# Optimization experiments

Measured on AMD Instinct MI355X. Metric: run time of the kernel, lower is better.

Reference implementation:

```python
import jax, jax.numpy as jnp
import numpy as np

H, G, D = 16, 4, 64  # heads, n_global, head_dim
DM = H * D           # 1024 hidden size
B, N = 8, 4096


def setup_inputs() -> dict:
    key = jax.random.key(0)
    ks = jax.random.split(key, 16)
    std = 0.02
    def lin(k, fi, fo):
        return jax.random.normal(k, (fi, fo), dtype=jnp.float32) * std
    return {
        "hidden_states": jax.random.normal(ks[0], (B, N, DM), dtype=jnp.float32),
        "attention_mask": jnp.zeros((B, 1, N), dtype=jnp.float32),
        "Wq": lin(ks[1], DM, DM), "bq": jnp.zeros((DM,), jnp.float32),
        "Wqa": lin(ks[2], DM, H * G), "bqa": jnp.zeros((H * G,), jnp.float32),
        "Wk": lin(ks[3], DM, DM), "bk": jnp.zeros((DM,), jnp.float32),
        "Wka": lin(ks[4], DM, H * G), "bka": jnp.zeros((H * G,), jnp.float32),
        "Wv": lin(ks[5], DM, DM), "bv": jnp.zeros((DM,), jnp.float32),
        "Wt": lin(ks[6], DM, DM), "bt": jnp.zeros((DM,), jnp.float32),
    }


def reference(hidden_states, attention_mask, Wq, bq, Wqa, bqa, Wk, bk, Wka, bka, Wv, bv, Wt, bt):
    b, n, _ = hidden_states.shape
    scale = D ** 0.5
    q = hidden_states @ Wq + bq            # b n (h d)
    k = hidden_states @ Wk + bk
    v = hidden_states @ Wv + bv
    # query attention scores: b n (h g) -> b h g n
    qs = (q @ Wqa + bqa).reshape(b, n, H, G).transpose(0, 2, 3, 1) / scale
    qs = qs + attention_mask[:, None]      # broadcast over h (and g)
    qw = jax.nn.softmax(qs, axis=-1)       # b h g n
    mq = q.reshape(b, n, H, D).transpose(0, 2, 1, 3)   # b h n d
    gq = jnp.einsum('bhgn,bhnd->bhdg', qw, mq)          # b h d g
    kh = k.reshape(b, n, H, D).transpose(0, 2, 1, 3)    # b h n d
    qk = kh[..., None] * gq[:, :, None]                 # b h n d g
    qk = qk.transpose(0, 2, 1, 3, 4).reshape(b, n, H * D, G)
    qk = jnp.max(qk, axis=-1)                           # b n (h d)
    # NOTE: original code adds mask but does NOT softmax this score
    ksc = (qk @ Wka + bka).reshape(b, n, H, G).transpose(0, 2, 3, 1) / scale
    ksc = ksc + attention_mask[:, None]                 # b h g n
    gk = jnp.einsum('bhgn,bhnd->bhdg', ksc, kh)         # b h d g
    vh = v.reshape(b, n, H, D).transpose(0, 2, 1, 3)    # b h n d
    u = gk[:, :, None] * vh[..., None]                  # b h n d g
    u = jnp.max(u, axis=-1)                             # b h n d
    u = u.transpose(0, 2, 1, 3).reshape(b, n, H * D)    # b n (h d)
    r = u @ Wt + bt
    return r + q
```

## Files before the change

kernel.cpp:

```cpp
#include <hip/hip_runtime.h>
#include <hip/hip_bf16.h>

typedef __bf16 bf16;
typedef __attribute__((ext_vector_type(8))) __bf16 bf16x8;
typedef __attribute__((ext_vector_type(4))) float floatx4;


__device__ __forceinline__ void gload_lds16(const void* g, void* l) {
    __builtin_amdgcn_global_load_lds(
        (const __attribute__((address_space(1))) unsigned int*)g,
        (__attribute__((address_space(3))) unsigned int*)l, 16, 0, 0);
}

__global__ __launch_bounds__(256)
void cvt_kernel(const float* __restrict__ src, bf16* __restrict__ dst, int n8) {
    int i8 = blockIdx.x * 256 + threadIdx.x;
    if (i8 >= n8) return;
    const float* s = src + (size_t)i8 * 8;
    float4 x = *(const float4*)s;
    float4 y = *(const float4*)(s + 4);
    bf16x8 o;
    o[0] = (bf16)x.x; o[1] = (bf16)x.y; o[2] = (bf16)x.z; o[3] = (bf16)x.w;
    o[4] = (bf16)y.x; o[5] = (bf16)y.y; o[6] = (bf16)y.z; o[7] = (bf16)y.w;
    *(bf16x8*)(dst + (size_t)i8 * 8) = o;
}

__global__ __launch_bounds__(256)
void transpose_cvt_kernel(const float* __restrict__ src, bf16* __restrict__ dst, int R, int C) {
    __shared__ bf16 tile[64][65];
    int tr0 = blockIdx.x * 64;
    int tc0 = blockIdx.y * 64;
    int tx = threadIdx.x & 63, ty = threadIdx.x >> 6;
#pragma unroll
    for (int j = 0; j < 16; j++) {
        int r = ty + j * 4;
        tile[tx][r] = (bf16)src[(size_t)(tr0 + r) * C + tc0 + tx];
    }
    __syncthreads();
#pragma unroll
    for (int j = 0; j < 16; j++) {
        int r = ty + j * 4;
        dst[(size_t)(tc0 + r) * R + tr0 + tx] = tile[r][tx];
    }
}

__global__ __launch_bounds__(256)
void biaspack_kernel(const float* __restrict__ bq, const float* __restrict__ bk,
                     const float* __restrict__ bv, float* __restrict__ biasf,
                     float* __restrict__ zbias) {
    int i = blockIdx.x * 256 + threadIdx.x;
    if (i < 1024)      biasf[i] = bq[i];
    else if (i < 2048) biasf[i] = bk[i - 1024];
    else if (i < 3072) biasf[i] = bv[i - 2048];
    else if (i < 3200) biasf[i] = 0.f;
    else if (i < 4224) zbias[i - 3200] = 0.f;
}

__global__ __launch_bounds__(64)
void compbias_kernel(const float* __restrict__ bq, const float* __restrict__ Wqa,
                     const float* __restrict__ bqa, float* __restrict__ out) {
    int j = threadIdx.x;
    float a = 0.f;
    for (int t = 0; t < 1024; t++) a += bq[t] * Wqa[(size_t)t * 64 + j];
    out[j] = a + bqa[j];
}

template<int BN, int WN, int EPI>
__global__ __launch_bounds__(WN * 128)
void gemm_kernel(const bf16* __restrict__ A, int lda,
                 const bf16* __restrict__ WT,
                 const float* __restrict__ bias,
                 void* __restrict__ Cout, int ldc,
                 const float* __restrict__ mask,
                 const bf16* __restrict__ qadd, int ldq,
                 int K) {
    constexpr int BM = 128;
    constexpr int NT = WN * 128;
    __shared__ bf16 As[BM * 32];
    __shared__ bf16 Bs[BN * 32];

    const int tid  = threadIdx.x;
    const int wid  = tid >> 6;
    const int lane = tid & 63;
    const int l16  = lane & 15;
    const int quad = lane >> 4;
    const int wm   = wid & 1;
    const int wn   = wid >> 1;
    const int m0   = blockIdx.x * BM;
    const int n0   = blockIdx.y * BN;

    floatx4 acc[4][4];
#pragma unroll
    for (int i = 0; i < 4; i++)
#pragma unroll
        for (int j = 0; j < 4; j++) acc[i][j] = (floatx4)0.0f;

    for (int k0 = 0; k0 < K; k0 += 32) {
        __syncthreads();
#pragma unroll
        for (int i = tid; i < BM * 4; i += NT) {
            const bf16* gp = A + (size_t)(m0 + (i >> 2)) * lda + k0 + (i & 3) * 8;
            gload_lds16(gp, (char*)As + (size_t)(i & ~63) * 16);
        }
#pragma unroll
        for (int i = tid; i < BN * 4; i += NT) {
            const bf16* gp = WT + (size_t)(n0 + (i >> 2)) * K + k0 + (i & 3) * 8;
            gload_lds16(gp, (char*)Bs + (size_t)(i & ~63) * 16);
        }
        __syncthreads();
        bf16x8 af[4], bfv[4];
#pragma unroll
        for (int mi = 0; mi < 4; mi++)
            af[mi] = *(const bf16x8*)&As[(wm * 64 + mi * 16 + l16) * 32 + quad * 8];
#pragma unroll
        for (int ni = 0; ni < 4; ni++)
            bfv[ni] = *(const bf16x8*)&Bs[(wn * 64 + ni * 16 + l16) * 32 + quad * 8];
#pragma unroll
        for (int mi = 0; mi < 4; mi++)
#pragma unroll
            for (int ni = 0; ni < 4; ni++)
                acc[mi][ni] = __builtin_amdgcn_mfma_f32_16x16x32_bf16(
                    af[mi], bfv[ni], acc[mi][ni], 0, 0, 0);
    }

#pragma unroll
    for (int mi = 0; mi < 4; mi++) {
#pragma unroll
        for (int ni = 0; ni < 4; ni++) {
            int col  = n0 + wn * 64 + ni * 16 + l16;
            int rowb = m0 + wm * 64 + mi * 16 + quad * 4;
            float bv = bias[col];
#pragma unroll
            for (int e = 0; e < 4; e++) {
                int row = rowb + e;
                float v = acc[mi][ni][e] + bv;
                if (EPI == 0) {
                    ((bf16*)Cout)[(size_t)row * ldc + col] = (bf16)v;
                } else if (EPI == 2) {
                    ((float*)Cout)[(size_t)row * ldc + col] = v * 0.125f + mask[row];
                } else {
                    v += (float)qadd[(size_t)row * ldq + col];
                    ((float*)Cout)[(size_t)row * ldc + col] = v;
                }
            }
        }
    }
}

__global__ __launch_bounds__(256)
void softmax_kernel(const bf16* __restrict__ qkv, const float* __restrict__ mask,
                    float* __restrict__ qw) {
    int bh = blockIdx.x;
    int b = bh >> 6, hg = bh & 63;
    int tid = threadIdx.x;
    float xs[16];
    float mx = -1e30f;
#pragma unroll
    for (int j = 0; j < 16; j++) {
        int n = tid + j * 256;
        float x = (float)qkv[(size_t)(b * 4096 + n) * 3200 + 3072 + hg] * 0.125f
                  + mask[b * 4096 + n];
        xs[j] = x;
        mx = fmaxf(mx, x);
    }
    __shared__ float red[256];
    red[tid] = mx;
    __syncthreads();
    for (int s = 128; s > 0; s >>= 1) {
        if (tid < s) red[tid] = fmaxf(red[tid], red[tid + s]);
        __syncthreads();
    }
    mx = red[0];
    __syncthreads();
    float sum = 0.f;
#pragma unroll
    for (int j = 0; j < 16; j++) { xs[j] = __expf(xs[j] - mx); sum += xs[j]; }
    red[tid] = sum;
    __syncthreads();
    for (int s = 128; s > 0; s >>= 1) {
        if (tid < s) red[tid] += red[tid + s];
        __syncthreads();
    }
    float inv = 1.0f / red[0];
#pragma unroll
    for (int j = 0; j < 16; j++)
        qw[(size_t)bh * 4096 + tid + j * 256] = xs[j] * inv;
}

__global__ __launch_bounds__(256)
void gq1_kernel(const float* __restrict__ qw, const bf16* __restrict__ qkv,
                float* __restrict__ part) {
    int bh = blockIdx.x, ch = blockIdx.y;
    int b = bh >> 4, h = bh & 15;
    int tid = threadIdx.x;
    int g = tid >> 6, d = tid & 63;
    const float* wrow = qw + ((size_t)(b * 64 + h * 4 + g)) * 4096 + ch * 256;
    const bf16* qcol  = qkv + (size_t)(b * 4096 + ch * 256) * 3200 + h * 64 + d;
    float a = 0.f;
#pragma unroll 8
    for (int n = 0; n < 256; n++)
        a += wrow[n] * (float)qcol[(size_t)n * 3200];
    part[(((size_t)bh * 16 + ch) * 4 + g) * 64 + d] = a;
}

__global__ __launch_bounds__(256)
void gk1_kernel(const float* __restrict__ ksc, const bf16* __restrict__ qkv,
                float* __restrict__ part) {
    int bh = blockIdx.x, ch = blockIdx.y;
    int b = bh >> 4, h = bh & 15;
    int tid = threadIdx.x;
    int g = tid >> 6, d = tid & 63;
    const float* sbase = ksc + (size_t)(b * 4096 + ch * 256) * 64 + h * 4 + g;
    const bf16* kcol   = qkv + (size_t)(b * 4096 + ch * 256) * 3200 + 1024 + h * 64 + d;
    float a = 0.f;
#pragma unroll 8
    for (int n = 0; n < 256; n++)
        a += sbase[(size_t)n * 64] * (float)kcol[(size_t)n * 3200];
    part[(((size_t)bh * 16 + ch) * 4 + g) * 64 + d] = a;
}

__global__ __launch_bounds__(256)
void gred_kernel(const float* __restrict__ part,
                 float* __restrict__ gmax, float* __restrict__ gmin) {
    int bh = blockIdx.x;
    int tid = threadIdx.x;
    int g = tid >> 6, d = tid & 63;
    float a = 0.f;
#pragma unroll
    for (int c = 0; c < 16; c++)
        a += part[(((size_t)bh * 16 + c) * 4 + g) * 64 + d];
    __shared__ float sg[4][64];
    sg[g][d] = a;
    __syncthreads();
    if (tid < 64) {
        float mx = sg[0][tid], mn = sg[0][tid];
#pragma unroll
        for (int gg = 1; gg < 4; gg++) {
            mx = fmaxf(mx, sg[gg][tid]);
            mn = fminf(mn, sg[gg][tid]);
        }
        gmax[bh * 64 + tid] = mx;
        gmin[bh * 64 + tid] = mn;
    }
}

__global__ __launch_bounds__(256)
void maxg_kernel(const bf16* __restrict__ qkv, int coloff,
                 const float* __restrict__ gmax, const float* __restrict__ gmin,
                 bf16* __restrict__ dst) {
    size_t i8 = (size_t)blockIdx.x * 256 + threadIdx.x;
    size_t e0 = i8 * 8;
    int row = (int)(e0 >> 10);
    int c   = (int)(e0 & 1023);
    int b   = row >> 12;
    bf16x8 kv = *(const bf16x8*)(qkv + (size_t)row * 3200 + coloff + c);
    bf16x8 out;
#pragma unroll
    for (int j = 0; j < 8; j++) {
        float f  = (float)kv[j];
        float gm = gmax[b * 1024 + c + j];
        float gn = gmin[b * 1024 + c + j];
        out[j] = (bf16)(f >= 0.f ? f * gm : f * gn);
    }
    *(bf16x8*)(dst + e0) = out;
}

extern "C" void kernel_launch(void* const* d_in, const int* in_sizes, int n_in,
                              void* d_out, int out_size, void* d_ws, size_t ws_size,
                              hipStream_t stream) {
    const float* hs   = (const float*)d_in[0];
    const float* mask = (const float*)d_in[1];
    const float* Wq   = (const float*)d_in[2];
    const float* bq   = (const float*)d_in[3];
    const float* Wqa  = (const float*)d_in[4];
    const float* bqa  = (const float*)d_in[5];
    const float* Wk   = (const float*)d_in[6];
    const float* bk   = (const float*)d_in[7];
    const float* Wka  = (const float*)d_in[8];
    const float* bka  = (const float*)d_in[9];
    const float* Wv   = (const float*)d_in[10];
    const float* bv   = (const float*)d_in[11];
    const float* Wt   = (const float*)d_in[12];
    const float* bt   = (const float*)d_in[13];

    char* p = (char*)d_ws;
    auto alloc = [&](size_t bytes) {
        char* r = p;
        p += (bytes + 255) & ~(size_t)255;
        return (void*)r;
    };
    bf16*  WT    = (bf16*) alloc((size_t)3200 * 1024 * 2);
    bf16*  WqBf  = (bf16*) alloc((size_t)1024 * 1024 * 2);
    bf16*  WqaT  = (bf16*) alloc((size_t)128 * 1024 * 2);
    bf16*  WkaT  = (bf16*) alloc((size_t)64 * 1024 * 2);
    bf16*  WtT   = (bf16*) alloc((size_t)1024 * 1024 * 2);
    float* biasf = (float*)alloc((size_t)3200 * 4);
    float* zbias = (float*)alloc((size_t)1024 * 4);
    bf16*  qkv   = (bf16*) alloc((size_t)32768 * 3200 * 2);
    bf16*  hsb   = (bf16*) alloc((size_t)32768 * 1024 * 2);
    float* qw    = (float*)alloc((size_t)512 * 4096 * 4);
    float* part  = (float*)alloc((size_t)128 * 16 * 256 * 4);
    float* gqmax = (float*)alloc((size_t)8192 * 4);
    float* gqmin = (float*)alloc((size_t)8192 * 4);
    float* gkmax = (float*)alloc((size_t)8192 * 4);
    float* gkmin = (float*)alloc((size_t)8192 * 4);
    bf16*  qk_u  = hsb;
    float* ksc   = qw;

    cvt_kernel<<<16384, 256, 0, stream>>>(hs, hsb, 4194304);
    cvt_kernel<<<512, 256, 0, stream>>>(Wq, WqBf, 131072);
    transpose_cvt_kernel<<<dim3(16, 16), 256, 0, stream>>>(Wq, WT, 1024, 1024);
    transpose_cvt_kernel<<<dim3(16, 16), 256, 0, stream>>>(Wk, WT + (size_t)1024 * 1024, 1024, 1024);
    transpose_cvt_kernel<<<dim3(16, 16), 256, 0, stream>>>(Wv, WT + (size_t)2048 * 1024, 1024, 1024);
    transpose_cvt_kernel<<<dim3(16, 1), 256, 0, stream>>>(Wqa, WqaT, 1024, 64);
    transpose_cvt_kernel<<<dim3(16, 1), 256, 0, stream>>>(Wka, WkaT, 1024, 64);
    transpose_cvt_kernel<<<dim3(16, 16), 256, 0, stream>>>(Wt, WtT, 1024, 1024);
    biaspack_kernel<<<17, 256, 0, stream>>>(bq, bk, bv, biasf, zbias);
    compbias_kernel<<<1, 64, 0, stream>>>(bq, Wqa, bqa, biasf + 3072);
    gemm_kernel<128, 2, 0><<<dim3(1, 8), 256, 0, stream>>>(
        WqaT, 1024, WqBf, zbias, WT + (size_t)3072 * 1024, 1024, nullptr, nullptr, 0, 1024);

    gemm_kernel<128, 2, 0><<<dim3(256, 25), 256, 0, stream>>>(
        hsb, 1024, WT, biasf, qkv, 3200, nullptr, nullptr, 0, 1024);
    softmax_kernel<<<512, 256, 0, stream>>>(qkv, mask, qw);
    gq1_kernel<<<dim3(128, 16), 256, 0, stream>>>(qw, qkv, part);
    gred_kernel<<<128, 256, 0, stream>>>(part, gqmax, gqmin);
    maxg_kernel<<<16384, 256, 0, stream>>>(qkv, 1024, gqmax, gqmin, qk_u);
    gemm_kernel<64, 1, 2><<<dim3(256, 1), 128, 0, stream>>>(
        qk_u, 1024, WkaT, bka, ksc, 64, mask, nullptr, 0, 1024);
    gk1_kernel<<<dim3(128, 16), 256, 0, stream>>>(ksc, qkv, part);
    gred_kernel<<<128, 256, 0, stream>>>(part, gkmax, gkmin);
    maxg_kernel<<<16384, 256, 0, stream>>>(qkv, 2048, gkmax, gkmin, qk_u);
    gemm_kernel<128, 2, 3><<<dim3(256, 8), 256, 0, stream>>>(
        qk_u, 1024, WtT, bt, d_out, 1024, nullptr, qkv, 3200, 1024);
}
```

Measured before the change: 988.2 us.

## Add 256x256 double-buffered MFMA GEMM with interleaved staging for big projections

Adds a new 512-thread GEMM kernel with 256x256 output tiles, 128KB of dynamic LDS double buffering, direct global-to-LDS loads interleaved between MFMA phases, explicit waitcnt and barriers, s_setprio around the MFMA blocks, and an XCD-aware block swizzle. It replaces the 128-tile GEMM for the fused QKV projection and for the output projection. The larger tiles raise data reuse and cut global traffic, and the schedule hides load latency. The QKV weight buffer is padded to 3328 rows because the N tiles overrun 3200 columns, and the padding rows are read but never initialised. The hand-written barrier and waitcnt schedule is fragile.

```diff
diff --git a/kernel.cpp b/kernel.cpp
--- a/kernel.cpp
+++ b/kernel.cpp
@@ -11,6 +11,9 @@
         (const __attribute__((address_space(1))) unsigned int*)g,
         (__attribute__((address_space(3))) unsigned int*)l, 16, 0, 0);
 }
+
+#define WAIT_LGKM0() asm volatile("s_waitcnt lgkmcnt(0)" ::: "memory")
+#define WAIT_VM(N) asm volatile("s_waitcnt vmcnt(" #N ")" ::: "memory")
 
 __global__ __launch_bounds__(256)
 void cvt_kernel(const float* __restrict__ src, bf16* __restrict__ dst, int n8) {
@@ -141,6 +144,163 @@
                 } else {
                     v += (float)qadd[(size_t)row * ldq + col];
                     ((float*)Cout)[(size_t)row * ldc + col] = v;
+                }
+            }
+        }
+    }
+}
+
+#define DO_MFMA(MH, NH)                                                              \
+    _Pragma("unroll")                                                                \
+    for (int r_ = 0; r_ < 4; ++r_) {                                                 \
+        _Pragma("unroll")                                                            \
+        for (int nj_ = 0; nj_ < 2; ++nj_) {                                          \
+            _Pragma("unroll")                                                        \
+            for (int kk_ = 0; kk_ < 2; ++kk_) {                                      \
+                acc[(MH) * 4 + r_][(NH) * 2 + nj_] =                                 \
+                    __builtin_amdgcn_mfma_f32_16x16x32_bf16(                         \
+                        af[r_][kk_], bfv[(NH) * 2 + nj_][kk_],                       \
+                        acc[(MH) * 4 + r_][(NH) * 2 + nj_], 0, 0, 0);                \
+            }                                                                        \
+        }                                                                            \
+    }
+
+template<int EPI>
+__global__ __launch_bounds__(512, 2)
+void gemm256_kernel(const bf16* __restrict__ A, int lda,
+                    const bf16* __restrict__ B, int ldb,
+                    const float* __restrict__ bias,
+                    void* __restrict__ Cout, int ldc, int ncols,
+                    const bf16* __restrict__ qadd, int ldq,
+                    int K, int ntn) {
+    extern __shared__ __align__(16) char smem[];
+    const int tid  = threadIdx.x;
+    const int wid  = tid >> 6;
+    const int lane = tid & 63;
+    const int l16  = lane & 15;
+    const int quad = lane >> 4;
+    const int wm   = wid >> 2;
+    const int wn   = wid & 3;
+
+    const int nwg  = gridDim.x * gridDim.y;
+    const int orig = blockIdx.y * gridDim.x + blockIdx.x;
+    int swz = orig;
+    if ((nwg & 7) == 0) swz = (orig & 7) * (nwg >> 3) + (orig >> 3);
+    const int m0 = (swz / ntn) * 256;
+    const int n0 = (swz % ntn) * 256;
+
+    const int NT = K >> 6;
+
+    const int lrow = lane >> 2;
+    const int lcb8 = ((lane & 3) ^ ((lane >> 5) << 1)) << 3;
+    const int aoff = (l16 * 64 + quad * 16) ^ ((l16 & 8) << 2);
+
+    auto stage = [&](const bf16* __restrict__ base, int ldx, int r0,
+                     int kt, int h, int lbase) {
+#pragma unroll
+        for (int j = 0; j < 2; ++j) {
+            int rg_l = j * 4 + (wid >> 1);
+            int cg   = wid & 1;
+            const bf16* gp = base + (size_t)(r0 + h * 128 + rg_l * 16 + lrow) * ldx
+                             + (kt << 6) + (cg << 5) + lcb8;
+            char* lp = smem + lbase + ((kt & 1) << 15)
+                       + (((h * 8 + rg_l) * 2 + cg) << 10);
+            gload_lds16(gp, lp);
+        }
+    };
+
+    floatx4 acc[8][4];
+#pragma unroll
+    for (int i = 0; i < 8; ++i)
+#pragma unroll
+        for (int j = 0; j < 4; ++j) acc[i][j] = (floatx4)0.0f;
+
+    stage(B, ldb, n0, 0, 0, 65536);
+    stage(B, ldb, n0, 0, 1, 65536);
+    stage(A, lda, m0, 0, 0, 0);
+    stage(A, lda, m0, 0, 1, 0);
+    stage(B, ldb, n0, 1, 0, 65536);
+    stage(B, ldb, n0, 1, 1, 65536);
+    WAIT_VM(4);
+    __builtin_amdgcn_s_barrier();
+
+    for (int t = 0; t < NT; ++t) {
+        const int bsel = (t & 1) << 15;
+        bf16x8 af[4][2], bfv[4][2];
+
+#pragma unroll
+        for (int r = 0; r < 4; ++r)
+#pragma unroll
+            for (int kk = 0; kk < 2; ++kk)
+                af[r][kk] = *(const bf16x8*)(smem + bsel
+                              + (((wm * 8 + r) * 2 + kk) << 10) + aoff);
+#pragma unroll
+        for (int ni = 0; ni < 4; ++ni)
+#pragma unroll
+            for (int kk = 0; kk < 2; ++kk)
+                bfv[ni][kk] = *(const bf16x8*)(smem + 65536 + bsel
+                              + (((wn * 4 + ni) * 2 + kk) << 10) + aoff);
+        if (t + 1 < NT) stage(A, lda, m0, t + 1, 0, 0);
+        __builtin_amdgcn_s_barrier();
+        WAIT_LGKM0();
+        __builtin_amdgcn_s_setprio(1);
+        DO_MFMA(0, 0)
+        __builtin_amdgcn_s_setprio(0);
+        __builtin_amdgcn_s_barrier();
+
+        if (t + 1 < NT) stage(A, lda, m0, t + 1, 1, 0);
+        __builtin_amdgcn_s_barrier();
+        __builtin_amdgcn_s_setprio(1);
+        DO_MFMA(0, 1)
+        __builtin_amdgcn_s_setprio(0);
+        __builtin_amdgcn_s_barrier();
+
+#pragma unroll
+        for (int r = 0; r < 4; ++r)
+#pragma unroll
+            for (int kk = 0; kk < 2; ++kk)
+                af[r][kk] = *(const bf16x8*)(smem + bsel
+                              + (((wm * 8 + 4 + r) * 2 + kk) << 10) + aoff);
+        if (t + 2 < NT) stage(B, ldb, n0, t + 2, 0, 65536);
+        __builtin_amdgcn_s_barrier();
+        WAIT_LGKM0();
+        __builtin_amdgcn_s_setprio(1);
+        DO_MFMA(1, 0)
+        __builtin_amdgcn_s_setprio(0);
+        __builtin_amdgcn_s_barrier();
+
+        if (t + 2 < NT) stage(B, ldb, n0, t + 2, 1, 65536);
+        __builtin_amdgcn_s_barrier();
+        __builtin_amdgcn_s_setprio(1);
+        DO_MFMA(1, 1)
+        __builtin_amdgcn_s_setprio(0);
+        if (t < NT - 2) {
+            WAIT_VM(4);
+            __builtin_amdgcn_s_barrier();
+        } else if (t == NT - 2) {
+            WAIT_VM(0);
+            __builtin_amdgcn_s_barrier();
+        }
+    }
+
+#pragma unroll
+    for (int mi = 0; mi < 8; ++mi) {
+#pragma unroll
+        for (int ni = 0; ni < 4; ++ni) {
+            int col  = n0 + wn * 64 + ni * 16 + l16;
+            int rowb = m0 + wm * 128 + mi * 16 + quad * 4;
+            if (col < ncols) {
+                float bv = bias[col];
+#pragma unroll
+                for (int e = 0; e < 4; ++e) {
+                    int row = rowb + e;
+                    float v = acc[mi][ni][e] + bv;
+                    if (EPI == 0) {
+                        ((bf16*)Cout)[(size_t)row * ldc + col] = (bf16)v;
+                    } else {
+                        v += (float)qadd[(size_t)row * ldq + col];
+                        ((float*)Cout)[(size_t)row * ldc + col] = v;
+                    }
                 }
             }
         }
@@ -289,7 +449,7 @@
         p += (bytes + 255) & ~(size_t)255;
         return (void*)r;
     };
-    bf16*  WT    = (bf16*) alloc((size_t)3200 * 1024 * 2);
+    bf16*  WT    = (bf16*) alloc((size_t)3328 * 1024 * 2);
     bf16*  WqBf  = (bf16*) alloc((size_t)1024 * 1024 * 2);
     bf16*  WqaT  = (bf16*) alloc((size_t)128 * 1024 * 2);
     bf16*  WkaT  = (bf16*) alloc((size_t)64 * 1024 * 2);
@@ -307,6 +467,11 @@
     bf16*  qk_u  = hsb;
     float* ksc   = qw;
 
+    (void)hipFuncSetAttribute(reinterpret_cast<const void*>(&gemm256_kernel<0>),
+                              hipFuncAttributeMaxDynamicSharedMemorySize, 131072);
+    (void)hipFuncSetAttribute(reinterpret_cast<const void*>(&gemm256_kernel<3>),
+                              hipFuncAttributeMaxDynamicSharedMemorySize, 131072);
+
     cvt_kernel<<<16384, 256, 0, stream>>>(hs, hsb, 4194304);
     cvt_kernel<<<512, 256, 0, stream>>>(Wq, WqBf, 131072);
     transpose_cvt_kernel<<<dim3(16, 16), 256, 0, stream>>>(Wq, WT, 1024, 1024);
@@ -320,8 +485,8 @@
     gemm_kernel<128, 2, 0><<<dim3(1, 8), 256, 0, stream>>>(
         WqaT, 1024, WqBf, zbias, WT + (size_t)3072 * 1024, 1024, nullptr, nullptr, 0, 1024);
 
-    gemm_kernel<128, 2, 0><<<dim3(256, 25), 256, 0, stream>>>(
-        hsb, 1024, WT, biasf, qkv, 3200, nullptr, nullptr, 0, 1024);
+    gemm256_kernel<0><<<dim3(128, 13), 512, 131072, stream>>>(
+        hsb, 1024, WT, 1024, biasf, qkv, 3200, 3200, nullptr, 0, 1024, 13);
     softmax_kernel<<<512, 256, 0, stream>>>(qkv, mask, qw);
     gq1_kernel<<<dim3(128, 16), 256, 0, stream>>>(qw, qkv, part);
     gred_kernel<<<128, 256, 0, stream>>>(part, gqmax, gqmin);
@@ -331,6 +496,6 @@
     gk1_kernel<<<dim3(128, 16), 256, 0, stream>>>(ksc, qkv, part);
     gred_kernel<<<128, 256, 0, stream>>>(part, gkmax, gkmin);
     maxg_kernel<<<16384, 256, 0, stream>>>(qkv, 2048, gkmax, gkmin, qk_u);
-    gemm_kernel<128, 2, 3><<<dim3(256, 8), 256, 0, stream>>>(
-        qk_u, 1024, WtT, bt, d_out, 1024, nullptr, qkv, 3200, 1024);
-}
+    gemm256_kernel<3><<<dim3(128, 4), 512, 131072, stream>>>(
+        qk_u, 1024, WtT, 1024, bt, d_out, 1024, 1024, qkv, 3200, 1024, 4);
+}
```

After: 936.0 us. 5.3% less time.

## Add 256x256-tile 8-wave pipelined GEMM for QKV and output projections

Applied to the files above, without the earlier changes.

Adds a new bf16 MFMA GEMM using 256x256 output tiles with 512 threads, a 4-stage LDS ring filled by direct global-to-LDS loads, interleaved half-tile MFMA with explicit vmcnt waits and barriers, setprio around compute, and an XCD-aware block swizzle. The two large projection GEMMs (QKV and final output) use it in place of the 128-tile kernel. The aim is more data reuse per tile and better overlap of loads with MFMA. The weight buffer is padded to 3328 rows so the 13th column tile can read past 3200, and stores are masked by column. Costs are 128KB of LDS per block and more registers, which limits occupancy.

```diff
diff --git a/kernel.cpp b/kernel.cpp
--- a/kernel.cpp
+++ b/kernel.cpp
@@ -11,6 +11,8 @@
         (const __attribute__((address_space(1))) unsigned int*)g,
         (__attribute__((address_space(3))) unsigned int*)l, 16, 0, 0);
 }
+
+#define WAIT_VM(N) asm volatile("s_waitcnt vmcnt(" #N ")" ::: "memory")
 
 __global__ __launch_bounds__(256)
 void cvt_kernel(const float* __restrict__ src, bf16* __restrict__ dst, int n8) {
@@ -141,6 +143,120 @@
                 } else {
                     v += (float)qadd[(size_t)row * ldq + col];
                     ((float*)Cout)[(size_t)row * ldc + col] = v;
+                }
+            }
+        }
+    }
+}
+
+#define STG_A(KT) do { \
+    gload_lds16(gA0 + (KT) * 32, sA + (((KT) & 3) << 14)); \
+    gload_lds16(gA1 + (KT) * 32, sA + (((KT) & 3) << 14) + 1024); } while (0)
+#define STG_B(KT) do { \
+    gload_lds16(gB0 + (KT) * 32, sB + (((KT) & 3) << 14)); \
+    gload_lds16(gB1 + (KT) * 32, sB + (((KT) & 3) << 14) + 1024); } while (0)
+#define RD_AFA(T) { _Pragma("unroll") for (int r_ = 0; r_ < 4; ++r_) \
+    af_a[r_] = *(const bf16x8*)(lA + (((T) & 3) << 14) + r_ * 1024); }
+#define RD_AFB(T) { _Pragma("unroll") for (int r_ = 0; r_ < 4; ++r_) \
+    af_b[r_] = *(const bf16x8*)(lA + (((T) & 3) << 14) + 4096 + r_ * 1024); }
+#define RD_BFV(T, S) { _Pragma("unroll") for (int n_ = 0; n_ < 4; ++n_) \
+    bfv[S][n_] = *(const bf16x8*)(lB + (((T) & 3) << 14) + n_ * 1024); }
+#define MM_HALF(MH, S) { _Pragma("unroll") for (int r_ = 0; r_ < 4; ++r_) \
+    _Pragma("unroll") for (int n_ = 0; n_ < 4; ++n_) \
+    acc[(MH) * 4 + r_][n_] = __builtin_amdgcn_mfma_f32_16x16x32_bf16( \
+        (MH) ? af_b[r_] : af_a[r_], bfv[S][n_], acc[(MH) * 4 + r_][n_], 0, 0, 0); }
+
+template<int EPI>
+__global__ __launch_bounds__(512, 2)
+void gemm256_kernel(const bf16* __restrict__ A, int lda,
+                    const bf16* __restrict__ B, int ldb,
+                    const float* __restrict__ bias,
+                    void* __restrict__ Cout, int ldc, int ncols,
+                    const bf16* __restrict__ qadd, int ldq,
+                    int ntn) {
+    constexpr int NT = 32;
+    extern __shared__ __align__(16) char smem[];
+    const int tid  = threadIdx.x;
+    const int wid  = tid >> 6;
+    const int lane = tid & 63;
+    const int l16  = lane & 15;
+    const int quad = lane >> 4;
+    const int wm   = wid >> 2;
+    const int wn   = wid & 3;
+
+    const int nwg  = gridDim.x * gridDim.y;
+    const int orig = blockIdx.y * gridDim.x + blockIdx.x;
+    int swz = orig;
+    if ((nwg & 7) == 0) swz = (orig & 7) * (nwg >> 3) + (orig >> 3);
+    const int m0 = (swz / ntn) * 256;
+    const int n0 = (swz % ntn) * 256;
+
+    const int srow = wid * 32 + (lane >> 2);
+    const int scol = ((lane & 3) ^ ((lane >> 5) << 1)) << 3;
+    const bf16* gA0 = A + (size_t)(m0 + srow) * lda + scol;
+    const bf16* gA1 = gA0 + (size_t)16 * lda;
+    const bf16* gB0 = B + (size_t)(n0 + srow) * ldb + scol;
+    const bf16* gB1 = gB0 + (size_t)16 * ldb;
+    char* sA = smem + wid * 2048;
+    char* sB = smem + 65536 + wid * 2048;
+    const int aoff = (l16 * 64 + quad * 16) ^ ((l16 & 8) << 2);
+    const char* lA = smem + wm * 8192 + aoff;
+    const char* lB = smem + 65536 + wn * 4096 + aoff;
+
+    floatx4 acc[8][4];
+#pragma unroll
+    for (int i = 0; i < 8; ++i)
+#pragma unroll
+        for (int j = 0; j < 4; ++j) acc[i][j] = (floatx4)0.0f;
+
+    bf16x8 af_a[4], af_b[4], bfv[2][4];
+
+    STG_A(0); STG_B(0); STG_A(1); STG_B(1); STG_A(2); STG_B(2);
+    WAIT_VM(8);
+    __builtin_amdgcn_s_barrier();
+    RD_AFA(0);
+    RD_BFV(0, 0);
+
+#pragma unroll
+    for (int t = 0; t < NT; ++t) {
+        RD_AFB(t);
+        if (t + 3 < NT) STG_A(t + 3);
+        __builtin_amdgcn_s_barrier();
+        __builtin_amdgcn_s_setprio(1);
+        MM_HALF(0, t & 1);
+        __builtin_amdgcn_s_setprio(0);
+        if (t < NT - 3)       { WAIT_VM(6); }
+        else if (t == NT - 3) { WAIT_VM(4); }
+        else if (t == NT - 2) { WAIT_VM(0); }
+        __builtin_amdgcn_s_barrier();
+
+        if (t + 1 < NT) { RD_AFA(t + 1); RD_BFV(t + 1, (t + 1) & 1); }
+        if (t + 3 < NT) STG_B(t + 3);
+        __builtin_amdgcn_s_barrier();
+        __builtin_amdgcn_s_setprio(1);
+        MM_HALF(1, t & 1);
+        __builtin_amdgcn_s_setprio(0);
+        __builtin_amdgcn_s_barrier();
+    }
+
+#pragma unroll
+    for (int mi = 0; mi < 8; ++mi) {
+#pragma unroll
+        for (int ni = 0; ni < 4; ++ni) {
+            int col  = n0 + wn * 64 + ni * 16 + l16;
+            int rowb = m0 + wm * 128 + mi * 16 + quad * 4;
+            if (col < ncols) {
+                float bv = bias[col];
+#pragma unroll
+                for (int e = 0; e < 4; ++e) {
+                    int row = rowb + e;
+                    float v = acc[mi][ni][e] + bv;
+                    if (EPI == 0) {
+                        ((bf16*)Cout)[(size_t)row * ldc + col] = (bf16)v;
+                    } else {
+                        v += (float)qadd[(size_t)row * ldq + col];
+                        ((float*)Cout)[(size_t)row * ldc + col] = v;
+                    }
                 }
             }
         }
@@ -289,7 +405,7 @@
         p += (bytes + 255) & ~(size_t)255;
         return (void*)r;
     };
-    bf16*  WT    = (bf16*) alloc((size_t)3200 * 1024 * 2);
+    bf16*  WT    = (bf16*) alloc((size_t)3328 * 1024 * 2);
     bf16*  WqBf  = (bf16*) alloc((size_t)1024 * 1024 * 2);
     bf16*  WqaT  = (bf16*) alloc((size_t)128 * 1024 * 2);
     bf16*  WkaT  = (bf16*) alloc((size_t)64 * 1024 * 2);
@@ -307,6 +423,11 @@
     bf16*  qk_u  = hsb;
     float* ksc   = qw;
 
+    (void)hipFuncSetAttribute(reinterpret_cast<const void*>(&gemm256_kernel<0>),
+                              hipFuncAttributeMaxDynamicSharedMemorySize, 131072);
+    (void)hipFuncSetAttribute(reinterpret_cast<const void*>(&gemm256_kernel<3>),
+                              hipFuncAttributeMaxDynamicSharedMemorySize, 131072);
+
     cvt_kernel<<<16384, 256, 0, stream>>>(hs, hsb, 4194304);
     cvt_kernel<<<512, 256, 0, stream>>>(Wq, WqBf, 131072);
     transpose_cvt_kernel<<<dim3(16, 16), 256, 0, stream>>>(Wq, WT, 1024, 1024);
@@ -320,8 +441,8 @@
     gemm_kernel<128, 2, 0><<<dim3(1, 8), 256, 0, stream>>>(
         WqaT, 1024, WqBf, zbias, WT + (size_t)3072 * 1024, 1024, nullptr, nullptr, 0, 1024);
 
-    gemm_kernel<128, 2, 0><<<dim3(256, 25), 256, 0, stream>>>(
-        hsb, 1024, WT, biasf, qkv, 3200, nullptr, nullptr, 0, 1024);
+    gemm256_kernel<0><<<dim3(128, 13), 512, 131072, stream>>>(
+        hsb, 1024, WT, 1024, biasf, qkv, 3200, 3200, nullptr, 0, 13);
     softmax_kernel<<<512, 256, 0, stream>>>(qkv, mask, qw);
     gq1_kernel<<<dim3(128, 16), 256, 0, stream>>>(qw, qkv, part);
     gred_kernel<<<128, 256, 0, stream>>>(part, gqmax, gqmin);
@@ -331,6 +452,6 @@
     gk1_kernel<<<dim3(128, 16), 256, 0, stream>>>(ksc, qkv, part);
     gred_kernel<<<128, 256, 0, stream>>>(part, gkmax, gkmin);
     maxg_kernel<<<16384, 256, 0, stream>>>(qkv, 2048, gkmax, gkmin, qk_u);
-    gemm_kernel<128, 2, 3><<<dim3(256, 8), 256, 0, stream>>>(
-        qk_u, 1024, WtT, bt, d_out, 1024, nullptr, qkv, 3200, 1024);
-}
+    gemm256_kernel<3><<<dim3(128, 4), 512, 131072, stream>>>(
+        qk_u, 1024, WtT, 1024, bt, d_out, 1024, 1024, qkv, 3200, 4);
+}
```

New measurement: 906.6 us. 8.3% less time.
